# Kernel optimization log

Measured on AMD Instinct MI355X. Metric: run time of the kernel, lower is better.

The kernel has to match this reference:

```python
import jax, jax.numpy as jnp
import numpy as np

B, S, D, H = 4, 2048, 1024, 16
NEG = -1e10  # matches the module's -10000000000.0 additive mask


def setup_inputs() -> dict:
    key = jax.random.key(0)
    k1, k2, k3, k4, k5 = jax.random.split(key, 5)
    scale = 0.02
    return {
        "x": jax.random.normal(k1, (B, S, D), dtype=jnp.float32),
        "w_qkv": jax.random.normal(k2, (D, 3 * D), dtype=jnp.float32) * scale,
        "b_qkv": jax.random.normal(k3, (3 * D,), dtype=jnp.float32) * scale,
        "w_out": jax.random.normal(k4, (D, D), dtype=jnp.float32) * scale,
        "b_out": jax.random.normal(k5, (D,), dtype=jnp.float32) * scale,
    }


def reference(x, w_qkv, b_qkv, w_out, b_out):
    b, s, d = x.shape
    hd = d // H  # per-head dim
    qkv = x @ w_qkv + b_qkv  # [b,s,3d]
    qq, kk, vv = jnp.split(qkv, 3, axis=-1)
    # [b,h,s,hd]
    qq = qq.reshape(b, s, H, hd).transpose(0, 2, 1, 3)
    kk = kk.reshape(b, s, H, hd).transpose(0, 2, 1, 3)
    vv = vv.reshape(b, s, H, hd).transpose(0, 2, 1, 3)
    scale = 1.0 / float(hd) ** 0.5
    # additive causal mask: NEG above diagonal, 0 on/below (as in module)
    mask = (1.0 - jnp.tri(s, dtype=jnp.float32)) * NEG
    attn = jnp.einsum("bhqd,bhkd->bhqk", qq, kk) * scale + mask
    attn = jax.nn.softmax(attn, axis=-1)
    out = jnp.einsum("bhqk,bhkd->bhqd", attn, vv)  # [b,h,s,hd]
    out = out.transpose(0, 2, 1, 3).reshape(b, s, d)
    return out @ w_out + b_out
```

## Files before the change

kernel.cpp:

```cpp
#include <hip/hip_runtime.h>
#include <hip/hip_bf16.h>
#include <stdint.h>


#define B_   4
#define S_   2048
#define D_   1024
#define H_   16
#define HD_  64
#define MTOK (B_ * S_)

typedef __attribute__((ext_vector_type(8))) short bfx8;
typedef __attribute__((ext_vector_type(4))) float fx4;

static __device__ __forceinline__ unsigned short f2bf(float f) {
    union { float f; uint32_t u; } v{f};
    uint32_t u = v.u;
    u += 0x7fffu + ((u >> 16) & 1u);
    return (unsigned short)(u >> 16);
}

static __device__ __forceinline__ uint32_t cvtpk(float lo, float hi) {
    uint32_t r;
    asm volatile("v_cvt_pk_bf16_f32 %0, %1, %2" : "=v"(r) : "v"(lo), "v"(hi));
    return r;
}

static __device__ __forceinline__ void gll16(const unsigned short* g, const unsigned short* l) {
    typedef const __attribute__((address_space(1))) void* gp_t;
    typedef __attribute__((address_space(3))) void* lp_t;
    __builtin_amdgcn_global_load_lds((gp_t)(uintptr_t)g, (lp_t)(uint32_t)(uintptr_t)l, 16, 0, 0);
}

__global__ void k_conv_x(const float* __restrict__ x, unsigned short* __restrict__ xb, int n8) {
    int i = blockIdx.x * blockDim.x + threadIdx.x;
    int stride = gridDim.x * blockDim.x;
    for (; i < n8; i += stride) {
        const float4* p = (const float4*)(x + (size_t)i * 8);
        float4 a = p[0], b = p[1];
        bfx8 o;
        o[0]=f2bf(a.x); o[1]=f2bf(a.y); o[2]=f2bf(a.z); o[3]=f2bf(a.w);
        o[4]=f2bf(b.x); o[5]=f2bf(b.y); o[6]=f2bf(b.z); o[7]=f2bf(b.w);
        *(bfx8*)(xb + (size_t)i * 8) = o;
    }
}

__global__ void k_transpose_bf(const float* __restrict__ w, unsigned short* __restrict__ wt,
                               int K, int N) {
    int idx = blockIdx.x * blockDim.x + threadIdx.x;
    int total = N * (K / 8);
    if (idx >= total) return;
    int n  = idx % N;
    int k0 = (idx / N) * 8;
    bfx8 o;
#pragma unroll
    for (int j = 0; j < 8; ++j) o[j] = f2bf(w[(size_t)(k0 + j) * N + n]);
    *(bfx8*)(wt + (size_t)n * K + k0) = o;
}

#define GBK 64
#define QSCALE 0.18033688011112042f

__launch_bounds__(256)
__global__ void k_gemm_qkv(const unsigned short* __restrict__ A,
                           const unsigned short* __restrict__ Bt,
                           const float* __restrict__ bias,
                           unsigned short* __restrict__ Qw,
                           unsigned short* __restrict__ Kw,
                           unsigned short* __restrict__ Vt) {
    __shared__ unsigned short Al[128 * GBK];
    __shared__ unsigned short Bl[128 * GBK];
    const int m0 = blockIdx.y * 128;
    const int n0 = blockIdx.x * 128;
    const int t = threadIdx.x;
    const int w = t >> 6, l = t & 63;
    const int wr = w >> 1, wc = w & 1;
    const int lr = l & 15, lg = l >> 4;
    const int srow = w * 32 + (l >> 3);
    const int scol = (l & 7) * 8;
    fx4 acc[4][4] = {};

    for (int k0 = 0; k0 < D_; k0 += GBK) {
        __syncthreads();
#pragma unroll
        for (int j = 0; j < 4; ++j) {
            gll16(&A [(size_t)(m0 + srow + j * 8) * D_ + k0 + scol], &Al[(w * 32 + j * 8) * GBK]);
            gll16(&Bt[(size_t)(n0 + srow + j * 8) * D_ + k0 + scol], &Bl[(w * 32 + j * 8) * GBK]);
        }
        __syncthreads();
#pragma unroll
        for (int kk = 0; kk < 2; ++kk) {
            bfx8 af[4], bf[4];
#pragma unroll
            for (int i = 0; i < 4; ++i) af[i] = *(const bfx8*)&Al[(wr * 64 + i * 16 + lr) * GBK + kk * 32 + lg * 8];
#pragma unroll
            for (int i = 0; i < 4; ++i) bf[i] = *(const bfx8*)&Bl[(wc * 64 + i * 16 + lr) * GBK + kk * 32 + lg * 8];
#pragma unroll
            for (int mi = 0; mi < 4; ++mi)
#pragma unroll
                for (int ni = 0; ni < 4; ++ni)
                    acc[mi][ni] = __builtin_amdgcn_mfma_f32_16x16x32_bf16(af[mi], bf[ni], acc[mi][ni], 0, 0, 0);
        }
    }

    const int colbase = n0 + wc * 64;
    const int mat = colbase >> 10;
#pragma unroll
    for (int ni = 0; ni < 4; ++ni) {
        int col = colbase + ni * 16 + lr;
        int dcol = col & 1023;
        int h = dcol >> 6, dd = dcol & 63;
        float bv = bias[col];
#pragma unroll
        for (int mi = 0; mi < 4; ++mi) {
#pragma unroll
            for (int i = 0; i < 4; ++i) {
                int m = m0 + wr * 64 + mi * 16 + lg * 4 + i;
                int b = m >> 11, s = m & 2047;
                float v = acc[mi][ni][i] + bv;
                int bh = b * H_ + h;
                if (mat == 0)      Qw[((size_t)bh * S_ + s) * HD_ + dd] = f2bf(v * QSCALE);
                else if (mat == 1) Kw[((size_t)bh * S_ + s) * HD_ + dd] = f2bf(v);
                else               Vt[((size_t)bh * HD_ + dd) * S_ + s] = f2bf(v);
            }
        }
    }
}

__launch_bounds__(512, 4)
__global__ void k_attn(const unsigned short* __restrict__ Qw,
                       const unsigned short* __restrict__ Kw,
                       const unsigned short* __restrict__ Vt,
                       unsigned short* __restrict__ Ob) {
    __shared__ unsigned short Kl[2][64 * 64];
    __shared__ unsigned short Vl[2][64 * 64];
    __shared__ unsigned short Pl[8][16 * 72];
    const int bh = blockIdx.y;
    const int pi = blockIdx.x;
    const int t = threadIdx.x;
    const int w = t >> 6, l = t & 63;
    const int lr = l & 15, lg = l >> 4;
    const int qA = pi * 128 + w * 16;
    const int qB = (15 - pi) * 128 + w * 16;
    const int NT = 32 - 2 * pi;

    const unsigned short* Qp = Qw + (size_t)bh * S_ * HD_;
    const unsigned short* Kp = Kw + (size_t)bh * S_ * HD_;
    const unsigned short* Vp = Vt + (size_t)bh * HD_ * S_;

    bfx8 qfA[2], qfB[2];
#pragma unroll
    for (int kk = 0; kk < 2; ++kk) {
        qfA[kk] = *(const bfx8*)&Qp[(size_t)(qA + lr) * HD_ + kk * 32 + lg * 8];
        qfB[kk] = *(const bfx8*)&Qp[(size_t)(qB + lr) * HD_ + kk * 32 + lg * 8];
    }

    fx4 oA[4] = {}, oB[4] = {};
    float mA = -1e30f, lA = 0.f, mB = -1e30f, lB = 0.f;

    auto compute = [&](int qr, const bfx8* qf, fx4* oacc, float& mrow, float& lsum,
                       int kv0, int buf) {
        fx4 sacc[4] = {};
#pragma unroll
        for (int c = 0; c < 4; ++c) {
            int row = c * 16 + lr;
#pragma unroll
            for (int kk = 0; kk < 2; ++kk) {
                int colb = kk * 64 + lg * 16;
                bfx8 kf = *(const bfx8*)((const char*)&Kl[buf][0] + row * 128 + (colb ^ ((row & 7) << 4)));
                sacc[c] = __builtin_amdgcn_mfma_f32_16x16x32_bf16(kf, qf[kk], sacc[c], 0, 0, 0);
            }
        }
        if (kv0 + 63 > qr) {
            const int qrel = qr + lr - kv0;
#pragma unroll
            for (int c = 0; c < 4; ++c)
#pragma unroll
                for (int i = 0; i < 4; ++i)
                    if (c * 16 + lg * 4 + i > qrel) sacc[c][i] = -1e30f;
        }
        float mc0 = fmaxf(fmaxf(sacc[0][0], sacc[0][1]), fmaxf(sacc[0][2], sacc[0][3]));
        float mc1 = fmaxf(fmaxf(sacc[1][0], sacc[1][1]), fmaxf(sacc[1][2], sacc[1][3]));
        float mc2 = fmaxf(fmaxf(sacc[2][0], sacc[2][1]), fmaxf(sacc[2][2], sacc[2][3]));
        float mc3 = fmaxf(fmaxf(sacc[3][0], sacc[3][1]), fmaxf(sacc[3][2], sacc[3][3]));
        float mx = fmaxf(fmaxf(mc0, mc1), fmaxf(mc2, mc3));
        mx = fmaxf(mx, __shfl_xor(mx, 16));
        mx = fmaxf(mx, __shfl_xor(mx, 32));
        float mnew = fmaxf(mrow, mx);
        float al = exp2f(mrow - mnew);
        mrow = mnew;
        float ps = 0.f;
        uint32_t pk[4][2];
#pragma unroll
        for (int c = 0; c < 4; ++c)
#pragma unroll
            for (int r = 0; r < 2; ++r) {
                float p0 = exp2f(sacc[c][2 * r]     - mnew);
                float p1 = exp2f(sacc[c][2 * r + 1] - mnew);
                ps += p0 + p1;
                pk[c][r] = cvtpk(p0, p1);
            }
        ps += __shfl_xor(ps, 16);
        ps += __shfl_xor(ps, 32);
        lsum = lsum * al + ps;
#pragma unroll
        for (int c = 0; c < 4; ++c) {
            uint2 u; u.x = pk[c][0]; u.y = pk[c][1];
            *(uint2*)&Pl[w][lr * 72 + c * 16 + lg * 4] = u;
        }
#pragma unroll
        for (int c = 0; c < 4; ++c)
#pragma unroll
            for (int i = 0; i < 4; ++i) oacc[c][i] *= al;
#pragma unroll
        for (int kk = 0; kk < 2; ++kk) {
            bfx8 pf = *(const bfx8*)&Pl[w][lr * 72 + kk * 32 + lg * 8];
#pragma unroll
            for (int c = 0; c < 4; ++c) {
                int vrow = c * 16 + lr;
                int vcolb = kk * 64 + lg * 16;
                bfx8 vf = *(const bfx8*)((const char*)&Vl[buf][0] + vrow * 128 + (vcolb ^ ((vrow & 7) << 4)));
                oacc[c] = __builtin_amdgcn_mfma_f32_16x16x32_bf16(vf, pf, oacc[c], 0, 0, 0);
            }
        }
    };

    {
        bfx8 sreg[2];
#pragma unroll
        for (int it = 0; it < 2; ++it) {
            int id = t + 512 * it;
            int c = id & 511;
            int row = c >> 3, q = c & 7;
            if (id < 512) sreg[it] = *(const bfx8*)&Kp[(size_t)row * HD_ + q * 8];
            else          sreg[it] = *(const bfx8*)&Vp[(size_t)row * S_ + q * 8];
        }
#pragma unroll
        for (int it = 0; it < 2; ++it) {
            int id = t + 512 * it;
            int c = id & 511;
            int row = c >> 3, q = c & 7;
            int off = row * 128 + ((q * 16) ^ ((row & 7) << 4));
            char* base = (id < 512) ? (char*)&Kl[0][0] : (char*)&Vl[0][0];
            *(bfx8*)(base + off) = sreg[it];
        }
    }
    __syncthreads();

    int buf = 0;
    for (int tkv = 0; tkv < NT; ++tkv) {
        const int kv0 = tkv * 64;
        const bool pre = (tkv + 1 < NT);
        bfx8 sreg[2];
        if (pre) {
            const int kn = kv0 + 64;
#pragma unroll
            for (int it = 0; it < 2; ++it) {
                int id = t + 512 * it;
                int c = id & 511;
                int row = c >> 3, q = c & 7;
                if (id < 512) sreg[it] = *(const bfx8*)&Kp[(size_t)(kn + row) * HD_ + q * 8];
                else          sreg[it] = *(const bfx8*)&Vp[(size_t)row * S_ + kn + q * 8];
            }
        }
        if (kv0 <= qB + 15) compute(qB, qfB, oB, mB, lB, kv0, buf);
        if (kv0 <= qA + 15) compute(qA, qfA, oA, mA, lA, kv0, buf);
        if (pre) {
#pragma unroll
            for (int it = 0; it < 2; ++it) {
                int id = t + 512 * it;
                int c = id & 511;
                int row = c >> 3, q = c & 7;
                int off = row * 128 + ((q * 16) ^ ((row & 7) << 4));
                char* base = (id < 512) ? (char*)&Kl[buf ^ 1][0] : (char*)&Vl[buf ^ 1][0];
                *(bfx8*)(base + off) = sreg[it];
            }
        }
        __syncthreads();
        buf ^= 1;
    }

    const int b = bh >> 4, h = bh & 15;
    const float ivA = __builtin_amdgcn_rcpf(lA);
    const float ivB = __builtin_amdgcn_rcpf(lB);
#pragma unroll
    for (int c = 0; c < 4; ++c) {
        uint2 ua, ub;
        ua.x = cvtpk(oA[c][0] * ivA, oA[c][1] * ivA);
        ua.y = cvtpk(oA[c][2] * ivA, oA[c][3] * ivA);
        ub.x = cvtpk(oB[c][0] * ivB, oB[c][1] * ivB);
        ub.y = cvtpk(oB[c][2] * ivB, oB[c][3] * ivB);
        int col = h * 64 + c * 16 + lg * 4;
        *(uint2*)&Ob[((size_t)b * S_ + qA + lr) * D_ + col] = ua;
        *(uint2*)&Ob[((size_t)b * S_ + qB + lr) * D_ + col] = ub;
    }
}

__launch_bounds__(256)
__global__ void k_gemm_proj(const unsigned short* __restrict__ A,
                            const unsigned short* __restrict__ Bt,
                            const float* __restrict__ bias,
                            float* __restrict__ out) {
    __shared__ unsigned short Al[128 * GBK];
    __shared__ unsigned short Bl[128 * GBK];
    const int m0 = blockIdx.y * 128;
    const int n0 = blockIdx.x * 128;
    const int t = threadIdx.x;
    const int w = t >> 6, l = t & 63;
    const int wr = w >> 1, wc = w & 1;
    const int lr = l & 15, lg = l >> 4;
    const int srow = w * 32 + (l >> 3);
    const int scol = (l & 7) * 8;
    fx4 acc[4][4] = {};

    for (int k0 = 0; k0 < D_; k0 += GBK) {
        __syncthreads();
#pragma unroll
        for (int j = 0; j < 4; ++j) {
            gll16(&A [(size_t)(m0 + srow + j * 8) * D_ + k0 + scol], &Al[(w * 32 + j * 8) * GBK]);
            gll16(&Bt[(size_t)(n0 + srow + j * 8) * D_ + k0 + scol], &Bl[(w * 32 + j * 8) * GBK]);
        }
        __syncthreads();
#pragma unroll
        for (int kk = 0; kk < 2; ++kk) {
            bfx8 af[4], bf[4];
#pragma unroll
            for (int i = 0; i < 4; ++i) af[i] = *(const bfx8*)&Al[(wr * 64 + i * 16 + lr) * GBK + kk * 32 + lg * 8];
#pragma unroll
            for (int i = 0; i < 4; ++i) bf[i] = *(const bfx8*)&Bl[(wc * 64 + i * 16 + lr) * GBK + kk * 32 + lg * 8];
#pragma unroll
            for (int mi = 0; mi < 4; ++mi)
#pragma unroll
                for (int ni = 0; ni < 4; ++ni)
                    acc[mi][ni] = __builtin_amdgcn_mfma_f32_16x16x32_bf16(af[mi], bf[ni], acc[mi][ni], 0, 0, 0);
        }
    }
#pragma unroll
    for (int ni = 0; ni < 4; ++ni) {
        int col = n0 + wc * 64 + ni * 16 + lr;
        float bv = bias[col];
#pragma unroll
        for (int mi = 0; mi < 4; ++mi)
#pragma unroll
            for (int i = 0; i < 4; ++i) {
                int m = m0 + wr * 64 + mi * 16 + lg * 4 + i;
                out[(size_t)m * D_ + col] = acc[mi][ni][i] + bv;
            }
    }
}

extern "C" void kernel_launch(void* const* d_in, const int* in_sizes, int n_in,
                              void* d_out, int out_size, void* d_ws, size_t ws_size,
                              hipStream_t stream) {
    const float* x     = (const float*)d_in[0];
    const float* w_qkv = (const float*)d_in[1];
    const float* b_qkv = (const float*)d_in[2];
    const float* w_out = (const float*)d_in[3];
    const float* b_out = (const float*)d_in[4];
    float* out = (float*)d_out;

    unsigned short* xb    = (unsigned short*)d_ws;
    unsigned short* wqkvT = xb    + (size_t)MTOK * D_;
    unsigned short* woutT = wqkvT + (size_t)3 * D_ * D_;
    unsigned short* Qw    = woutT + (size_t)D_ * D_;
    unsigned short* Kw    = Qw    + (size_t)MTOK * D_;
    unsigned short* Vt    = Kw    + (size_t)MTOK * D_;
    unsigned short* attnb = Vt    + (size_t)MTOK * D_;

    k_conv_x<<<2048, 256, 0, stream>>>(x, xb, MTOK * D_ / 8);
    k_transpose_bf<<<(3 * D_ * (D_ / 8)) / 256, 256, 0, stream>>>(w_qkv, wqkvT, D_, 3 * D_);
    k_transpose_bf<<<(D_ * (D_ / 8)) / 256, 256, 0, stream>>>(w_out, woutT, D_, D_);
    k_gemm_qkv<<<dim3(24, 64), 256, 0, stream>>>(xb, wqkvT, b_qkv, Qw, Kw, Vt);
    k_attn<<<dim3(8, B_ * H_), 512, 0, stream>>>(Qw, Kw, Vt, attnb);
    k_gemm_proj<<<dim3(8, 64), 256, 0, stream>>>(attnb, woutT, b_out, out);
}
```

Measured before the change: 236.0 us.

## Vectorize GEMM epilogues, add XCD-aware block mapping, split V transpose into kernel

The two GEMMs move to a K-step of 32 and swap the MFMA operand order, so each lane holds four consecutive columns. This lets the epilogues write packed bf16 or float4 stores instead of scattered scalar stores. V is now written row-major and transposed by a separate LDS-tiled kernel into the xb buffer, which is no longer needed, replacing the strided column scatter. Grids are flattened, with a remap that groups tiles and heads per XCD to improve L2 locality. The cost is an extra kernel launch and extra V traffic, plus twice as many barriers per K in the GEMMs.

```diff
diff --git a/kernel.cpp b/kernel.cpp
--- a/kernel.cpp
+++ b/kernel.cpp
@@ -9,6 +9,8 @@
 #define H_   16
 #define HD_  64
 #define MTOK (B_ * S_)
+#define BK   32
+#define QSCALE 0.18033688011112042f
 
 typedef __attribute__((ext_vector_type(8))) short bfx8;
 typedef __attribute__((ext_vector_type(4))) float fx4;
@@ -58,8 +60,30 @@
     *(bfx8*)(wt + (size_t)n * K + k0) = o;
 }
 
-#define GBK 64
-#define QSCALE 0.18033688011112042f
+__global__ void k_transpose_v(const unsigned short* __restrict__ Vw,
+                              unsigned short* __restrict__ Vt) {
+    __shared__ unsigned short lds[64][72];
+    const int bg = blockIdx.x;
+    const int bh = bg >> 5;
+    const int st = (bg & 31) * 64;
+    const int t = threadIdx.x;
+#pragma unroll
+    for (int j = 0; j < 2; ++j) {
+        int c = t + 256 * j;
+        int row = c >> 3, q = c & 7;
+        *(bfx8*)&lds[row][q * 8] = *(const bfx8*)&Vw[((size_t)bh * S_ + st + row) * HD_ + q * 8];
+    }
+    __syncthreads();
+#pragma unroll
+    for (int j = 0; j < 2; ++j) {
+        int c = t + 256 * j;
+        int d = c >> 3, q = c & 7;
+        bfx8 o;
+#pragma unroll
+        for (int e = 0; e < 8; ++e) o[e] = lds[q * 8 + e][d];
+        *(bfx8*)&Vt[((size_t)bh * HD_ + d) * S_ + st + q * 8] = o;
+    }
+}
 
 __launch_bounds__(256)
 __global__ void k_gemm_qkv(const unsigned short* __restrict__ A,
@@ -67,62 +91,61 @@
                            const float* __restrict__ bias,
                            unsigned short* __restrict__ Qw,
                            unsigned short* __restrict__ Kw,
-                           unsigned short* __restrict__ Vt) {
-    __shared__ unsigned short Al[128 * GBK];
-    __shared__ unsigned short Bl[128 * GBK];
-    const int m0 = blockIdx.y * 128;
-    const int n0 = blockIdx.x * 128;
+                           unsigned short* __restrict__ Vw) {
+    __shared__ unsigned short Al[128 * BK];
+    __shared__ unsigned short Bl[128 * BK];
+    const int wg = blockIdx.x;
+    const int lin = (wg & 7) * 192 + (wg >> 3);
+    const int ny = lin / 24, nx = lin - ny * 24;
+    const int m0 = ny * 128;
+    const int n0 = nx * 128;
     const int t = threadIdx.x;
     const int w = t >> 6, l = t & 63;
     const int wr = w >> 1, wc = w & 1;
     const int lr = l & 15, lg = l >> 4;
-    const int srow = w * 32 + (l >> 3);
-    const int scol = (l & 7) * 8;
+    const int srow = l >> 2;
+    const int scol = (l & 3) * 8;
     fx4 acc[4][4] = {};
 
-    for (int k0 = 0; k0 < D_; k0 += GBK) {
+    for (int k0 = 0; k0 < D_; k0 += BK) {
         __syncthreads();
 #pragma unroll
-        for (int j = 0; j < 4; ++j) {
-            gll16(&A [(size_t)(m0 + srow + j * 8) * D_ + k0 + scol], &Al[(w * 32 + j * 8) * GBK]);
-            gll16(&Bt[(size_t)(n0 + srow + j * 8) * D_ + k0 + scol], &Bl[(w * 32 + j * 8) * GBK]);
+        for (int j = 0; j < 2; ++j) {
+            int rb = j * 64 + w * 16;
+            gll16(&A [(size_t)(m0 + rb + srow) * D_ + k0 + scol], &Al[rb * BK]);
+            gll16(&Bt[(size_t)(n0 + rb + srow) * D_ + k0 + scol], &Bl[rb * BK]);
         }
         __syncthreads();
-#pragma unroll
-        for (int kk = 0; kk < 2; ++kk) {
-            bfx8 af[4], bf[4];
-#pragma unroll
-            for (int i = 0; i < 4; ++i) af[i] = *(const bfx8*)&Al[(wr * 64 + i * 16 + lr) * GBK + kk * 32 + lg * 8];
-#pragma unroll
-            for (int i = 0; i < 4; ++i) bf[i] = *(const bfx8*)&Bl[(wc * 64 + i * 16 + lr) * GBK + kk * 32 + lg * 8];
-#pragma unroll
-            for (int mi = 0; mi < 4; ++mi)
-#pragma unroll
-                for (int ni = 0; ni < 4; ++ni)
-                    acc[mi][ni] = __builtin_amdgcn_mfma_f32_16x16x32_bf16(af[mi], bf[ni], acc[mi][ni], 0, 0, 0);
-        }
-    }
-
-    const int colbase = n0 + wc * 64;
-    const int mat = colbase >> 10;
+        bfx8 af[4], bf[4];
+#pragma unroll
+        for (int i = 0; i < 4; ++i) af[i] = *(const bfx8*)&Al[(wr * 64 + i * 16 + lr) * BK + lg * 8];
+#pragma unroll
+        for (int i = 0; i < 4; ++i) bf[i] = *(const bfx8*)&Bl[(wc * 64 + i * 16 + lr) * BK + lg * 8];
+#pragma unroll
+        for (int mi = 0; mi < 4; ++mi)
+#pragma unroll
+            for (int ni = 0; ni < 4; ++ni)
+                acc[mi][ni] = __builtin_amdgcn_mfma_f32_16x16x32_bf16(bf[ni], af[mi], acc[mi][ni], 0, 0, 0);
+    }
+
 #pragma unroll
     for (int ni = 0; ni < 4; ++ni) {
-        int col = colbase + ni * 16 + lr;
-        int dcol = col & 1023;
-        int h = dcol >> 6, dd = dcol & 63;
-        float bv = bias[col];
+        const int nn = n0 + wc * 64 + ni * 16 + lg * 4;
+        const int mat = nn >> 10;
+        const int h = (nn & 1023) >> 6, dd = nn & 63;
+        const float4 bv = *(const float4*)&bias[nn];
+        unsigned short* dst = (mat == 0) ? Qw : (mat == 1) ? Kw : Vw;
+        const float sc = (mat == 0) ? QSCALE : 1.0f;
 #pragma unroll
         for (int mi = 0; mi < 4; ++mi) {
-#pragma unroll
-            for (int i = 0; i < 4; ++i) {
-                int m = m0 + wr * 64 + mi * 16 + lg * 4 + i;
-                int b = m >> 11, s = m & 2047;
-                float v = acc[mi][ni][i] + bv;
-                int bh = b * H_ + h;
-                if (mat == 0)      Qw[((size_t)bh * S_ + s) * HD_ + dd] = f2bf(v * QSCALE);
-                else if (mat == 1) Kw[((size_t)bh * S_ + s) * HD_ + dd] = f2bf(v);
-                else               Vt[((size_t)bh * HD_ + dd) * S_ + s] = f2bf(v);
-            }
+            const int m = m0 + wr * 64 + mi * 16 + lr;
+            const int b = m >> 11, s = m & 2047;
+            const int bh = b * H_ + h;
+            fx4 v = acc[mi][ni];
+            float o0 = (v[0] + bv.x) * sc, o1 = (v[1] + bv.y) * sc;
+            float o2 = (v[2] + bv.z) * sc, o3 = (v[3] + bv.w) * sc;
+            uint2 u; u.x = cvtpk(o0, o1); u.y = cvtpk(o2, o3);
+            *(uint2*)&dst[((size_t)bh * S_ + s) * HD_ + dd] = u;
         }
     }
 }
@@ -135,8 +158,10 @@
     __shared__ unsigned short Kl[2][64 * 64];
     __shared__ unsigned short Vl[2][64 * 64];
     __shared__ unsigned short Pl[8][16 * 72];
-    const int bh = blockIdx.y;
-    const int pi = blockIdx.x;
+    const int wg = blockIdx.x;
+    const int xcd = wg & 7, ix = wg >> 3;
+    const int bh = xcd * 8 + (ix >> 3);
+    const int pi = ix & 7;
     const int t = threadIdx.x;
     const int w = t >> 6, l = t & 63;
     const int lr = l & 15, lg = l >> 4;
@@ -301,51 +326,52 @@
                             const unsigned short* __restrict__ Bt,
                             const float* __restrict__ bias,
                             float* __restrict__ out) {
-    __shared__ unsigned short Al[128 * GBK];
-    __shared__ unsigned short Bl[128 * GBK];
-    const int m0 = blockIdx.y * 128;
-    const int n0 = blockIdx.x * 128;
+    __shared__ unsigned short Al[128 * BK];
+    __shared__ unsigned short Bl[128 * BK];
+    const int wg = blockIdx.x;
+    const int lin = (wg & 7) * 64 + (wg >> 3);
+    const int ny = lin >> 3, nx = lin & 7;
+    const int m0 = ny * 128;
+    const int n0 = nx * 128;
     const int t = threadIdx.x;
     const int w = t >> 6, l = t & 63;
     const int wr = w >> 1, wc = w & 1;
     const int lr = l & 15, lg = l >> 4;
-    const int srow = w * 32 + (l >> 3);
-    const int scol = (l & 7) * 8;
+    const int srow = l >> 2;
+    const int scol = (l & 3) * 8;
     fx4 acc[4][4] = {};
 
-    for (int k0 = 0; k0 < D_; k0 += GBK) {
+    for (int k0 = 0; k0 < D_; k0 += BK) {
         __syncthreads();
 #pragma unroll
-        for (int j = 0; j < 4; ++j) {
-            gll16(&A [(size_t)(m0 + srow + j * 8) * D_ + k0 + scol], &Al[(w * 32 + j * 8) * GBK]);
-            gll16(&Bt[(size_t)(n0 + srow + j * 8) * D_ + k0 + scol], &Bl[(w * 32 + j * 8) * GBK]);
+        for (int j = 0; j < 2; ++j) {
+            int rb = j * 64 + w * 16;
+            gll16(&A [(size_t)(m0 + rb + srow) * D_ + k0 + scol], &Al[rb * BK]);
+            gll16(&Bt[(size_t)(n0 + rb + srow) * D_ + k0 + scol], &Bl[rb * BK]);
         }
         __syncthreads();
-#pragma unroll
-        for (int kk = 0; kk < 2; ++kk) {
-            bfx8 af[4], bf[4];
-#pragma unroll
-            for (int i = 0; i < 4; ++i) af[i] = *(const bfx8*)&Al[(wr * 64 + i * 16 + lr) * GBK + kk * 32 + lg * 8];
-#pragma unroll
-            for (int i = 0; i < 4; ++i) bf[i] = *(const bfx8*)&Bl[(wc * 64 + i * 16 + lr) * GBK + kk * 32 + lg * 8];
-#pragma unroll
-            for (int mi = 0; mi < 4; ++mi)
-#pragma unroll
-                for (int ni = 0; ni < 4; ++ni)
-                    acc[mi][ni] = __builtin_amdgcn_mfma_f32_16x16x32_bf16(af[mi], bf[ni], acc[mi][ni], 0, 0, 0);
-        }
+        bfx8 af[4], bf[4];
+#pragma unroll
+        for (int i = 0; i < 4; ++i) af[i] = *(const bfx8*)&Al[(wr * 64 + i * 16 + lr) * BK + lg * 8];
+#pragma unroll
+        for (int i = 0; i < 4; ++i) bf[i] = *(const bfx8*)&Bl[(wc * 64 + i * 16 + lr) * BK + lg * 8];
+#pragma unroll
+        for (int mi = 0; mi < 4; ++mi)
+#pragma unroll
+            for (int ni = 0; ni < 4; ++ni)
+                acc[mi][ni] = __builtin_amdgcn_mfma_f32_16x16x32_bf16(bf[ni], af[mi], acc[mi][ni], 0, 0, 0);
     }
 #pragma unroll
     for (int ni = 0; ni < 4; ++ni) {
-        int col = n0 + wc * 64 + ni * 16 + lr;
-        float bv = bias[col];
-#pragma unroll
-        for (int mi = 0; mi < 4; ++mi)
-#pragma unroll
-            for (int i = 0; i < 4; ++i) {
-                int m = m0 + wr * 64 + mi * 16 + lg * 4 + i;
-                out[(size_t)m * D_ + col] = acc[mi][ni][i] + bv;
-            }
+        const int nn = n0 + wc * 64 + ni * 16 + lg * 4;
+        const float4 bv = *(const float4*)&bias[nn];
+#pragma unroll
+        for (int mi = 0; mi < 4; ++mi) {
+            const int m = m0 + wr * 64 + mi * 16 + lr;
+            fx4 v = acc[mi][ni];
+            float4 o; o.x = v[0] + bv.x; o.y = v[1] + bv.y; o.z = v[2] + bv.z; o.w = v[3] + bv.w;
+            *(float4*)&out[(size_t)m * D_ + nn] = o;
+        }
     }
 }
 
@@ -364,13 +390,15 @@
     unsigned short* woutT = wqkvT + (size_t)3 * D_ * D_;
     unsigned short* Qw    = woutT + (size_t)D_ * D_;
     unsigned short* Kw    = Qw    + (size_t)MTOK * D_;
-    unsigned short* Vt    = Kw    + (size_t)MTOK * D_;
-    unsigned short* attnb = Vt    + (size_t)MTOK * D_;
+    unsigned short* Vw    = Kw    + (size_t)MTOK * D_;
+    unsigned short* attnb = Vw    + (size_t)MTOK * D_;
+    unsigned short* Vt    = xb;
 
     k_conv_x<<<2048, 256, 0, stream>>>(x, xb, MTOK * D_ / 8);
     k_transpose_bf<<<(3 * D_ * (D_ / 8)) / 256, 256, 0, stream>>>(w_qkv, wqkvT, D_, 3 * D_);
     k_transpose_bf<<<(D_ * (D_ / 8)) / 256, 256, 0, stream>>>(w_out, woutT, D_, D_);
-    k_gemm_qkv<<<dim3(24, 64), 256, 0, stream>>>(xb, wqkvT, b_qkv, Qw, Kw, Vt);
-    k_attn<<<dim3(8, B_ * H_), 512, 0, stream>>>(Qw, Kw, Vt, attnb);
-    k_gemm_proj<<<dim3(8, 64), 256, 0, stream>>>(attnb, woutT, b_out, out);
-}
+    k_gemm_qkv<<<1536, 256, 0, stream>>>(xb, wqkvT, b_qkv, Qw, Kw, Vw);
+    k_transpose_v<<<2048, 256, 0, stream>>>(Vw, Vt);
+    k_attn<<<512, 512, 0, stream>>>(Qw, Kw, Vt, attnb);
+    k_gemm_proj<<<512, 256, 0, stream>>>(attnb, woutT, b_out, out);
+}
```

New measurement: 213.1 us. -9.7%, faster.
